# Kernel optimization log

Hardware: AMD Instinct MI355X
Metric: run time of the kernel (lower is better)

## Reference

```python
import jax, jax.numpy as jnp
import numpy as np

H = 10  # hidden_dim

def _lstm_layer(x_tbd, w_ih, w_hh, b_ih, b_hh):
    # x_tbd: [T, B, D]; w_ih: [4H, D]; w_hh: [4H, H]; biases [4H]
    B = x_tbd.shape[1]
    h0 = jnp.zeros((B, H), x_tbd.dtype)
    c0 = jnp.zeros((B, H), x_tbd.dtype)
    # precompute input projections for all timesteps: [T, B, 4H]
    xg = jnp.einsum('tbd,gd->tbg', x_tbd, w_ih) + b_ih + b_hh

    def step(carry, xg_t):
        h, c = carry
        gates = xg_t + h @ w_hh.T  # [B, 4H]
        i, f, g, o = jnp.split(gates, 4, axis=-1)  # torch gate order i,f,g,o
        i = jax.nn.sigmoid(i); f = jax.nn.sigmoid(f)
        g = jnp.tanh(g); o = jax.nn.sigmoid(o)
        c = f * c + i * g
        h = o * jnp.tanh(c)
        return (h, c), h

    (hT, cT), hs = jax.lax.scan(step, (h0, c0), xg)
    return hs, hT  # hs: [T, B, H]

def setup_inputs() -> dict:
    key = jax.random.key(0)
    ks = jax.random.split(key, 11)
    B, T, D = 32768, 28, 28
    s0 = 1.0 / np.sqrt(H)
    u = lambda k, shape: jax.random.uniform(k, shape, jnp.float32, -s0, s0)
    return {
        'x': jax.random.normal(ks[0], (B, T, D), jnp.float32),
        'w_ih0': u(ks[1], (4 * H, D)),
        'w_hh0': u(ks[2], (4 * H, H)),
        'b_ih0': u(ks[3], (4 * H,)),
        'b_hh0': u(ks[4], (4 * H,)),
        'w_ih1': u(ks[5], (4 * H, H)),
        'w_hh1': u(ks[6], (4 * H, H)),
        'b_ih1': u(ks[7], (4 * H,)),
        'b_hh1': u(ks[8], (4 * H,)),
        'w_cls': u(ks[9], (10, H)),
        'b_cls': u(ks[10], (10,)),
    }

def reference(x, w_ih0, w_hh0, b_ih0, b_hh0, w_ih1, w_hh1, b_ih1, b_hh1, w_cls, b_cls):
    x_tbd = jnp.swapaxes(x, 0, 1)  # [T, B, D]
    hs0, _ = _lstm_layer(x_tbd, w_ih0, w_hh0, b_ih0, b_hh0)
    _, hT1 = _lstm_layer(hs0, w_ih1, w_hh1, b_ih1, b_hh1)  # hT1 = h_n[-1]
    return hT1 @ w_cls.T + b_cls  # [B, 10]
```

## Files before the change

### kernel.cpp

```cpp
#include <hip/hip_runtime.h>


#define HDIM 10
#define DDIM 28
#define TSTEPS 28

typedef const __attribute__((address_space(1))) unsigned int gu32;
typedef __attribute__((address_space(3))) unsigned int lu32;

__device__ __forceinline__ void gld_lds16(const float* g, float4* l) {
    __builtin_amdgcn_global_load_lds((gu32*)g, (lu32*)l, 16, 0, 0);
}

__device__ __forceinline__ float fast_sigmoid(float v) {
    return __builtin_amdgcn_rcpf(1.0f + __expf(-v));
}
__device__ __forceinline__ float fast_tanh(float v) {
    return 2.0f * __builtin_amdgcn_rcpf(1.0f + __expf(-2.0f * v)) - 1.0f;
}

__global__ __launch_bounds__(512, 2) void lstm2_cls_kernel(
    const float* __restrict__ x,
    const float* __restrict__ w_ih0, const float* __restrict__ w_hh0,
    const float* __restrict__ b_ih0, const float* __restrict__ b_hh0,
    const float* __restrict__ w_ih1, const float* __restrict__ w_hh1,
    const float* __restrict__ b_ih1, const float* __restrict__ b_hh1,
    const float* __restrict__ w_cls, const float* __restrict__ b_cls,
    float* __restrict__ out)
{
    __shared__ float4 sx[2][7 * 64];
    __shared__ float g0[40 * 64];
    __shared__ float g1[40 * 64];
    __shared__ float wW0[40 * 40];
    __shared__ float wW1[40 * 20];
    __shared__ float sb0[40], sb1[40];

    const int tid  = threadIdx.x;
    const int lane = tid & 63;
    const int wid  = __builtin_amdgcn_readfirstlane(tid >> 6);
    const int b0   = blockIdx.x * 64;
    const int sample = b0 + lane;

    const int q     = wid >> 1;
    const int rbase = q * 10 + (wid & 1) * 5;
    const bool is_g = (q == 2);

    const float* xs = x + (size_t)sample * (TSTEPS * DDIM);

    if (wid < 7) gld_lds16(xs + 4 * wid, &sx[0][wid * 64 + lane]);

    for (int i = tid; i < 40 * 40; i += 512) {
        const int r = i / 40, c = i - r * 40;
        float v = 0.0f;
        if (c < DDIM)             v = w_ih0[r * DDIM + c];
        else if (c < DDIM + HDIM) v = w_hh0[r * HDIM + (c - DDIM)];
        wW0[i] = v;
    }
    for (int i = tid; i < 40 * 20; i += 512) {
        const int r = i / 20, c = i - r * 20;
        wW1[i] = (c < HDIM) ? w_ih1[r * HDIM + c] : w_hh1[r * HDIM + (c - HDIM)];
    }
    for (int i = tid; i < 40; i += 512) {
        sb0[i] = b_ih0[i] + b_hh0[i];
        sb1[i] = b_ih1[i] + b_hh1[i];
    }

    float h0[HDIM], c0[HDIM], h1[HDIM], c1[HDIM];
    #pragma unroll
    for (int u = 0; u < HDIM; ++u) { h0[u] = c0[u] = h1[u] = c1[u] = 0.0f; }

    __syncthreads();

    float bias0[5], bias1[5];
    #pragma unroll
    for (int k = 0; k < 5; ++k) {
        bias0[k] = sb0[rbase + k];
        bias1[k] = sb1[rbase + k];
    }

    #pragma unroll 1
    for (int t = 0; t < TSTEPS; ++t) {
        const int cur = t & 1;

        if (t + 1 < TSTEPS && wid < 7)
            gld_lds16(xs + (t + 1) * DDIM + 4 * wid, &sx[cur ^ 1][wid * 64 + lane]);

        float xr[DDIM];
        #pragma unroll
        for (int v = 0; v < 7; ++v) {
            const float4 qv = sx[cur][v * 64 + lane];
            xr[4*v+0] = qv.x; xr[4*v+1] = qv.y; xr[4*v+2] = qv.z; xr[4*v+3] = qv.w;
        }

        #pragma unroll
        for (int k = 0; k < 5; ++k) {
            const float4* wp = (const float4*)&wW0[(rbase + k) * 40];
            float acc = bias0[k];
            #pragma unroll
            for (int v = 0; v < 7; ++v) {
                const float4 w = wp[v];
                acc += xr[4*v+0]*w.x + xr[4*v+1]*w.y + xr[4*v+2]*w.z + xr[4*v+3]*w.w;
            }
            { const float4 w = wp[7]; acc += h0[0]*w.x + h0[1]*w.y + h0[2]*w.z + h0[3]*w.w; }
            { const float4 w = wp[8]; acc += h0[4]*w.x + h0[5]*w.y + h0[6]*w.z + h0[7]*w.w; }
            { const float4 w = wp[9]; acc += h0[8]*w.x + h0[9]*w.y; }
            g0[(rbase + k) * 64 + lane] = is_g ? fast_tanh(acc) : fast_sigmoid(acc);
        }
        __syncthreads();

        #pragma unroll
        for (int u = 0; u < HDIM; ++u) {
            const float iv = g0[(     u) * 64 + lane];
            const float fv = g0[(10 + u) * 64 + lane];
            const float gv = g0[(20 + u) * 64 + lane];
            const float ov = g0[(30 + u) * 64 + lane];
            const float c  = fv * c0[u] + iv * gv;
            c0[u] = c;
            h0[u] = ov * fast_tanh(c);
        }

        #pragma unroll
        for (int k = 0; k < 5; ++k) {
            const float4* wp = (const float4*)&wW1[(rbase + k) * 20];
            float acc = bias1[k];
            { const float4 w = wp[0]; acc += h0[0]*w.x + h0[1]*w.y + h0[2]*w.z + h0[3]*w.w; }
            { const float4 w = wp[1]; acc += h0[4]*w.x + h0[5]*w.y + h0[6]*w.z + h0[7]*w.w; }
            { const float4 w = wp[2]; acc += h0[8]*w.x + h0[9]*w.y + h1[0]*w.z + h1[1]*w.w; }
            { const float4 w = wp[3]; acc += h1[2]*w.x + h1[3]*w.y + h1[4]*w.z + h1[5]*w.w; }
            { const float4 w = wp[4]; acc += h1[6]*w.x + h1[7]*w.y + h1[8]*w.z + h1[9]*w.w; }
            g1[(rbase + k) * 64 + lane] = is_g ? fast_tanh(acc) : fast_sigmoid(acc);
        }
        __syncthreads();

        #pragma unroll
        for (int u = 0; u < HDIM; ++u) {
            const float iv = g1[(     u) * 64 + lane];
            const float fv = g1[(10 + u) * 64 + lane];
            const float gv = g1[(20 + u) * 64 + lane];
            const float ov = g1[(30 + u) * 64 + lane];
            const float c  = fv * c1[u] + iv * gv;
            c1[u] = c;
            h1[u] = ov * fast_tanh(c);
        }
    }

    if (wid < 2) {
        #pragma unroll
        for (int k = 0; k < 5; ++k) {
            const int o = wid * 5 + k;
            float a = b_cls[o];
            const float* wc = w_cls + o * HDIM;
            #pragma unroll
            for (int j = 0; j < HDIM; ++j) a += h1[j] * wc[j];
            out[(size_t)sample * 10 + o] = a;
        }
    }
}

extern "C" void kernel_launch(void* const* d_in, const int* in_sizes, int n_in,
                              void* d_out, int out_size, void* d_ws, size_t ws_size,
                              hipStream_t stream) {
    const float* x     = (const float*)d_in[0];
    const float* w_ih0 = (const float*)d_in[1];
    const float* w_hh0 = (const float*)d_in[2];
    const float* b_ih0 = (const float*)d_in[3];
    const float* b_hh0 = (const float*)d_in[4];
    const float* w_ih1 = (const float*)d_in[5];
    const float* w_hh1 = (const float*)d_in[6];
    const float* b_ih1 = (const float*)d_in[7];
    const float* b_hh1 = (const float*)d_in[8];
    const float* w_cls = (const float*)d_in[9];
    const float* b_cls = (const float*)d_in[10];
    float* out = (float*)d_out;

    const int B = in_sizes[0] / (TSTEPS * DDIM);
    const int grid = B / 64;

    hipLaunchKernelGGL(lstm2_cls_kernel, dim3(grid), dim3(512), 0, stream,
                       x, w_ih0, w_hh0, b_ih0, b_hh0,
                       w_ih1, w_hh1, b_ih1, b_hh1,
                       w_cls, b_cls, out);
}
```

Before: 283.2 us.

## Process two samples per thread to amortize weight LDS reads and barriers

Each block now handles 128 samples instead of 64, and every thread computes gate rows for two samples (A and B). Each LDS weight fetch and each barrier is now shared across twice as many samples, and the grid is halved. In exchange, register pressure roughly doubles, so launch bounds drop to one block per CU-slot, which lowers occupancy and latency hiding for the serial recurrence.

Result: slower. 322.2 us (+13.8%).

```diff
diff --git a/kernel.cpp b/kernel.cpp
--- a/kernel.cpp
+++ b/kernel.cpp
@@ -4,6 +4,7 @@
 #define HDIM 10
 #define DDIM 28
 #define TSTEPS 28
+#define SPB 128
 
 typedef const __attribute__((address_space(1))) unsigned int gu32;
 typedef __attribute__((address_space(3))) unsigned int lu32;
@@ -19,7 +20,7 @@
     return 2.0f * __builtin_amdgcn_rcpf(1.0f + __expf(-2.0f * v)) - 1.0f;
 }
 
-__global__ __launch_bounds__(512, 2) void lstm2_cls_kernel(
+__global__ __launch_bounds__(512, 1) void lstm2_cls_kernel(
     const float* __restrict__ x,
     const float* __restrict__ w_ih0, const float* __restrict__ w_hh0,
     const float* __restrict__ b_ih0, const float* __restrict__ b_hh0,
@@ -28,9 +29,9 @@
     const float* __restrict__ w_cls, const float* __restrict__ b_cls,
     float* __restrict__ out)
 {
-    __shared__ float4 sx[2][7 * 64];
-    __shared__ float g0[40 * 64];
-    __shared__ float g1[40 * 64];
+    __shared__ float4 sx[2][7 * SPB];
+    __shared__ float g0[40 * SPB];
+    __shared__ float g1[40 * SPB];
     __shared__ float wW0[40 * 40];
     __shared__ float wW1[40 * 20];
     __shared__ float sb0[40], sb1[40];
@@ -38,16 +39,21 @@
     const int tid  = threadIdx.x;
     const int lane = tid & 63;
     const int wid  = __builtin_amdgcn_readfirstlane(tid >> 6);
-    const int b0   = blockIdx.x * 64;
-    const int sample = b0 + lane;
+    const int b0   = blockIdx.x * SPB;
+    const int sA   = b0 + lane;
+    const int sB   = sA + 64;
 
     const int q     = wid >> 1;
     const int rbase = q * 10 + (wid & 1) * 5;
     const bool is_g = (q == 2);
 
-    const float* xs = x + (size_t)sample * (TSTEPS * DDIM);
-
-    if (wid < 7) gld_lds16(xs + 4 * wid, &sx[0][wid * 64 + lane]);
+    const float* xsA = x + (size_t)sA * (TSTEPS * DDIM);
+    const float* xsB = x + (size_t)sB * (TSTEPS * DDIM);
+
+    if (wid < 7) {
+        gld_lds16(xsA + 4 * wid, &sx[0][wid * SPB + lane]);
+        gld_lds16(xsB + 4 * wid, &sx[0][wid * SPB + 64 + lane]);
+    }
 
     for (int i = tid; i < 40 * 40; i += 512) {
         const int r = i / 40, c = i - r * 40;
@@ -65,9 +71,13 @@
         sb1[i] = b_ih1[i] + b_hh1[i];
     }
 
-    float h0[HDIM], c0[HDIM], h1[HDIM], c1[HDIM];
+    float h0A[HDIM], c0A[HDIM], h1A[HDIM], c1A[HDIM];
+    float h0B[HDIM], c0B[HDIM], h1B[HDIM], c1B[HDIM];
     #pragma unroll
-    for (int u = 0; u < HDIM; ++u) { h0[u] = c0[u] = h1[u] = c1[u] = 0.0f; }
+    for (int u = 0; u < HDIM; ++u) {
+        h0A[u] = c0A[u] = h1A[u] = c1A[u] = 0.0f;
+        h0B[u] = c0B[u] = h1B[u] = c1B[u] = 0.0f;
+    }
 
     __syncthreads();
 
@@ -82,65 +92,92 @@
     for (int t = 0; t < TSTEPS; ++t) {
         const int cur = t & 1;
 
-        if (t + 1 < TSTEPS && wid < 7)
-            gld_lds16(xs + (t + 1) * DDIM + 4 * wid, &sx[cur ^ 1][wid * 64 + lane]);
-
-        float xr[DDIM];
+        if (t + 1 < TSTEPS && wid < 7) {
+            gld_lds16(xsA + (t + 1) * DDIM + 4 * wid, &sx[cur ^ 1][wid * SPB + lane]);
+            gld_lds16(xsB + (t + 1) * DDIM + 4 * wid, &sx[cur ^ 1][wid * SPB + 64 + lane]);
+        }
+
+        float4 xA[7], xB[7];
         #pragma unroll
         for (int v = 0; v < 7; ++v) {
-            const float4 qv = sx[cur][v * 64 + lane];
-            xr[4*v+0] = qv.x; xr[4*v+1] = qv.y; xr[4*v+2] = qv.z; xr[4*v+3] = qv.w;
+            xA[v] = sx[cur][v * SPB + lane];
+            xB[v] = sx[cur][v * SPB + 64 + lane];
         }
 
         #pragma unroll
         for (int k = 0; k < 5; ++k) {
             const float4* wp = (const float4*)&wW0[(rbase + k) * 40];
-            float acc = bias0[k];
+            float aA = bias0[k], aB = bias0[k];
             #pragma unroll
             for (int v = 0; v < 7; ++v) {
                 const float4 w = wp[v];
-                acc += xr[4*v+0]*w.x + xr[4*v+1]*w.y + xr[4*v+2]*w.z + xr[4*v+3]*w.w;
+                aA += xA[v].x*w.x + xA[v].y*w.y + xA[v].z*w.z + xA[v].w*w.w;
+                aB += xB[v].x*w.x + xB[v].y*w.y + xB[v].z*w.z + xB[v].w*w.w;
             }
-            { const float4 w = wp[7]; acc += h0[0]*w.x + h0[1]*w.y + h0[2]*w.z + h0[3]*w.w; }
-            { const float4 w = wp[8]; acc += h0[4]*w.x + h0[5]*w.y + h0[6]*w.z + h0[7]*w.w; }
-            { const float4 w = wp[9]; acc += h0[8]*w.x + h0[9]*w.y; }
-            g0[(rbase + k) * 64 + lane] = is_g ? fast_tanh(acc) : fast_sigmoid(acc);
+            { const float4 w = wp[7];
+              aA += h0A[0]*w.x + h0A[1]*w.y + h0A[2]*w.z + h0A[3]*w.w;
+              aB += h0B[0]*w.x + h0B[1]*w.y + h0B[2]*w.z + h0B[3]*w.w; }
+            { const float4 w = wp[8];
+              aA += h0A[4]*w.x + h0A[5]*w.y + h0A[6]*w.z + h0A[7]*w.w;
+              aB += h0B[4]*w.x + h0B[5]*w.y + h0B[6]*w.z + h0B[7]*w.w; }
+            { const float4 w = wp[9];
+              aA += h0A[8]*w.x + h0A[9]*w.y;
+              aB += h0B[8]*w.x + h0B[9]*w.y; }
+            const int gi = (rbase + k) * SPB + lane;
+            g0[gi]      = is_g ? fast_tanh(aA) : fast_sigmoid(aA);
+            g0[gi + 64] = is_g ? fast_tanh(aB) : fast_sigmoid(aB);
         }
         __syncthreads();
 
         #pragma unroll
         for (int u = 0; u < HDIM; ++u) {
-            const float iv = g0[(     u) * 64 + lane];
-            const float fv = g0[(10 + u) * 64 + lane];
-            const float gv = g0[(20 + u) * 64 + lane];
-            const float ov = g0[(30 + u) * 64 + lane];
-            const float c  = fv * c0[u] + iv * gv;
-            c0[u] = c;
-            h0[u] = ov * fast_tanh(c);
+            const int gi = u * SPB + lane;
+            { const float iv = g0[gi], fv = g0[10*SPB + gi],
+                          gv = g0[20*SPB + gi], ov = g0[30*SPB + gi];
+              const float c = fv * c0A[u] + iv * gv;
+              c0A[u] = c; h0A[u] = ov * fast_tanh(c); }
+            { const float iv = g0[gi+64], fv = g0[10*SPB + gi+64],
+                          gv = g0[20*SPB + gi+64], ov = g0[30*SPB + gi+64];
+              const float c = fv * c0B[u] + iv * gv;
+              c0B[u] = c; h0B[u] = ov * fast_tanh(c); }
         }
 
         #pragma unroll
         for (int k = 0; k < 5; ++k) {
             const float4* wp = (const float4*)&wW1[(rbase + k) * 20];
-            float acc = bias1[k];
-            { const float4 w = wp[0]; acc += h0[0]*w.x + h0[1]*w.y + h0[2]*w.z + h0[3]*w.w; }
-            { const float4 w = wp[1]; acc += h0[4]*w.x + h0[5]*w.y + h0[6]*w.z + h0[7]*w.w; }
-            { const float4 w = wp[2]; acc += h0[8]*w.x + h0[9]*w.y + h1[0]*w.z + h1[1]*w.w; }
-            { const float4 w = wp[3]; acc += h1[2]*w.x + h1[3]*w.y + h1[4]*w.z + h1[5]*w.w; }
-            { const float4 w = wp[4]; acc += h1[6]*w.x + h1[7]*w.y + h1[8]*w.z + h1[9]*w.w; }
-            g1[(rbase + k) * 64 + lane] = is_g ? fast_tanh(acc) : fast_sigmoid(acc);
+            float aA = bias1[k], aB = bias1[k];
+            { const float4 w = wp[0];
+              aA += h0A[0]*w.x + h0A[1]*w.y + h0A[2]*w.z + h0A[3]*w.w;
+              aB += h0B[0]*w.x + h0B[1]*w.y + h0B[2]*w.z + h0B[3]*w.w; }
+            { const float4 w = wp[1];
+              aA += h0A[4]*w.x + h0A[5]*w.y + h0A[6]*w.z + h0A[7]*w.w;
+              aB += h0B[4]*w.x + h0B[5]*w.y + h0B[6]*w.z + h0B[7]*w.w; }
+            { const float4 w = wp[2];
+              aA += h0A[8]*w.x + h0A[9]*w.y + h1A[0]*w.z + h1A[1]*w.w;
+              aB += h0B[8]*w.x + h0B[9]*w.y + h1B[0]*w.z + h1B[1]*w.w; }
+            { const float4 w = wp[3];
+              aA += h1A[2]*w.x + h1A[3]*w.y + h1A[4]*w.z + h1A[5]*w.w;
+              aB += h1B[2]*w.x + h1B[3]*w.y + h1B[4]*w.z + h1B[5]*w.w; }
+            { const float4 w = wp[4];
+              aA += h1A[6]*w.x + h1A[7]*w.y + h1A[8]*w.z + h1A[9]*w.w;
+              aB += h1B[6]*w.x + h1B[7]*w.y + h1B[8]*w.z + h1B[9]*w.w; }
+            const int gi = (rbase + k) * SPB + lane;
+            g1[gi]      = is_g ? fast_tanh(aA) : fast_sigmoid(aA);
+            g1[gi + 64] = is_g ? fast_tanh(aB) : fast_sigmoid(aB);
         }
         __syncthreads();
 
         #pragma unroll
         for (int u = 0; u < HDIM; ++u) {
-            const float iv = g1[(     u) * 64 + lane];
-            const float fv = g1[(10 + u) * 64 + lane];
-            const float gv = g1[(20 + u) * 64 + lane];
-            const float ov = g1[(30 + u) * 64 + lane];
-            const float c  = fv * c1[u] + iv * gv;
-            c1[u] = c;
-            h1[u] = ov * fast_tanh(c);
+            const int gi = u * SPB + lane;
+            { const float iv = g1[gi], fv = g1[10*SPB + gi],
+                          gv = g1[20*SPB + gi], ov = g1[30*SPB + gi];
+              const float c = fv * c1A[u] + iv * gv;
+              c1A[u] = c; h1A[u] = ov * fast_tanh(c); }
+            { const float iv = g1[gi+64], fv = g1[10*SPB + gi+64],
+                          gv = g1[20*SPB + gi+64], ov = g1[30*SPB + gi+64];
+              const float c = fv * c1B[u] + iv * gv;
+              c1B[u] = c; h1B[u] = ov * fast_tanh(c); }
         }
     }
 
@@ -148,11 +185,15 @@
         #pragma unroll
         for (int k = 0; k < 5; ++k) {
             const int o = wid * 5 + k;
-            float a = b_cls[o];
             const float* wc = w_cls + o * HDIM;
+            float aA = b_cls[o], aB = b_cls[o];
             #pragma unroll
-            for (int j = 0; j < HDIM; ++j) a += h1[j] * wc[j];
-            out[(size_t)sample * 10 + o] = a;
+            for (int j = 0; j < HDIM; ++j) {
+                aA += h1A[j] * wc[j];
+                aB += h1B[j] * wc[j];
+            }
+            out[(size_t)sA * 10 + o] = aA;
+            out[(size_t)sB * 10 + o] = aB;
         }
     }
 }
@@ -174,7 +215,7 @@
     float* out = (float*)d_out;
 
     const int B = in_sizes[0] / (TSTEPS * DDIM);
-    const int grid = B / 64;
+    const int grid = B / SPB;
 
     hipLaunchKernelGGL(lstm2_cls_kernel, dim3(grid), dim3(512), 0, stream,
                        x, w_ih0, w_hh0, b_ih0, b_hh0,
```
